# Kernel optimization log

Hardware: AMD Instinct MI355X
Metric: run time of the kernel (lower is better)

The kernel has to match this reference:

```python
import jax, jax.numpy as jnp
import numpy as np

# B=batch, S=seq_len, E=events per example, H=hidden, V=vocab
B, S, E, H, V = 16, 512, 32, 768, 50265


def setup_inputs() -> dict:
    key = jax.random.key(0)
    ks = jax.random.split(key, 12)
    batch_arg = jax.random.randint(ks[0], (B, S), 0, V)
    # distinct event positions per row (the torch loop visits each event once)
    event_pos = jax.vmap(lambda k: jax.random.permutation(k, S)[:E])(
        jax.random.split(ks[1], B))
    mask_indices = event_pos[:, 0]  # ensure the extracted token saw the fusion
    sent_emb = jax.random.normal(ks[2], (B, E, H), dtype=jnp.float32)
    type_emb = jax.random.normal(ks[3], (B, S, H), dtype=jnp.float32)
    emb_table = jax.random.normal(ks[4], (V, H), dtype=jnp.float32) * 0.02
    W1_1 = jax.random.normal(ks[5], (H, H), dtype=jnp.float32) * 0.02
    W1_2 = jax.random.normal(ks[6], (H, H), dtype=jnp.float32) * 0.02
    W2_1 = jax.random.normal(ks[7], (H, H), dtype=jnp.float32) * 0.02
    W2_2 = jax.random.normal(ks[8], (H, H), dtype=jnp.float32) * 0.02
    lm_W = jax.random.normal(ks[9], (H, V), dtype=jnp.float32) * 0.02
    lm_b = jnp.zeros((V,), dtype=jnp.float32)
    return dict(batch_arg=batch_arg, event_pos=event_pos,
                mask_indices=mask_indices, sent_emb=sent_emb,
                type_emb=type_emb, emb_table=emb_table,
                W1_1=W1_1, W1_2=W1_2, W2_1=W2_1, W2_2=W2_2,
                lm_W=lm_W, lm_b=lm_b)


def reference(batch_arg, event_pos, mask_indices, sent_emb, type_emb,
              emb_table, W1_1, W1_2, W2_1, W2_2, lm_W, lm_b):
    # word embedding lookup: [B,S,H]
    word_emb = emb_table[batch_arg]
    bidx = jnp.arange(B)[:, None]
    # gather per-event instance / type embeddings: [B,E,H]
    inst = word_emb[bidx, event_pos]
    typ = type_emb[bidx, event_pos]
    # gate 1: fuse instance with sentence embedding
    g1 = jax.nn.sigmoid(inst @ W1_1 + sent_emb @ W1_2)
    o1 = g1 * inst + (1.0 - g1) * sent_emb
    # gate 2: fuse with type embedding
    g2 = jax.nn.sigmoid(o1 @ W2_1 + typ @ W2_2)
    o2 = g2 * o1 + (1.0 - g2) * typ
    # scatter fused embeddings back into word_emb (positions are distinct)
    word_emb = word_emb.at[bidx, event_pos].set(o2)
    # extract mask-token embedding per example, project to vocab (lm_head)
    mask_emb = word_emb[jnp.arange(B), mask_indices]  # [B,H]
    prediction = mask_emb @ lm_W + lm_b  # [B,V]
    return prediction
```

## Files before the change

### kernel.cpp

```cpp
#include <hip/hip_runtime.h>

#define Hn 768
#define Bn 16
#define Sn 512
#define En 32
#define Vn 50265

#define WPB 8
#define KPW (Hn / WPB)
#define VPB 128
#define CH  4

__global__ __launch_bounds__(256) void gate_layer1(
    const int* __restrict__ batch_arg, const int* __restrict__ event_pos,
    const int* __restrict__ mask_indices, const float* __restrict__ sent_emb,
    const float* __restrict__ emb_table, const float* __restrict__ W1_1,
    const float* __restrict__ W1_2, float* __restrict__ o1_out)
{
    const int b  = blockIdx.x;
    const int j0 = threadIdx.x & 63;
    const int ks = threadIdx.x >> 6;
    const int j  = blockIdx.y * 64 + j0;

    const int mask = mask_indices[b];
    int estar = -1;
    #pragma unroll
    for (int e = 0; e < En; ++e)
        if (event_pos[b * En + e] == mask && estar < 0) estar = e;
    const int tok = batch_arg[b * Sn + mask];

    __shared__ __align__(16) float s_inst[Hn];
    __shared__ __align__(16) float s_sent[Hn];
    for (int t = threadIdx.x; t < Hn; t += 256) {
        s_inst[t] = emb_table[(size_t)tok * Hn + t];
        s_sent[t] = (estar >= 0) ? sent_emb[((size_t)b * En + estar) * Hn + t] : 0.f;
    }
    __syncthreads();

    float a0 = 0.f, a1 = 0.f, c0 = 0.f, c1 = 0.f;
    const float* __restrict__ w1 = W1_1 + (size_t)ks * 192 * Hn + j;
    const float* __restrict__ w2 = W1_2 + (size_t)ks * 192 * Hn + j;
    const float4* __restrict__ si = (const float4*)(s_inst + ks * 192);
    const float4* __restrict__ ss = (const float4*)(s_sent + ks * 192);
    #pragma unroll 4
    for (int k4 = 0; k4 < 48; ++k4) {
        const float4 iv = si[k4];
        const float4 sv = ss[k4];
        const float* __restrict__ wa = w1 + (size_t)k4 * 4 * Hn;
        const float* __restrict__ wb = w2 + (size_t)k4 * 4 * Hn;
        a0 = fmaf(iv.x, wa[0],      a0);
        a1 = fmaf(iv.y, wa[Hn],     a1);
        a0 = fmaf(iv.z, wa[2 * Hn], a0);
        a1 = fmaf(iv.w, wa[3 * Hn], a1);
        c0 = fmaf(sv.x, wb[0],      c0);
        c1 = fmaf(sv.y, wb[Hn],     c1);
        c0 = fmaf(sv.z, wb[2 * Hn], c0);
        c1 = fmaf(sv.w, wb[3 * Hn], c1);
    }

    __shared__ float r_a[4][64];
    __shared__ float r_c[4][64];
    r_a[ks][j0] = a0 + a1; r_c[ks][j0] = c0 + c1;
    __syncthreads();
    if (ks == 0) {
        const float A = r_a[0][j0] + r_a[1][j0] + r_a[2][j0] + r_a[3][j0];
        const float C = r_c[0][j0] + r_c[1][j0] + r_c[2][j0] + r_c[3][j0];
        const float g = 1.f / (1.f + expf(-(A + C)));
        o1_out[b * Hn + j] = g * s_inst[j] + (1.f - g) * s_sent[j];
    }
}

__global__ __launch_bounds__(256) void gate_layer2(
    const int* __restrict__ batch_arg, const int* __restrict__ event_pos,
    const int* __restrict__ mask_indices, const float* __restrict__ type_emb,
    const float* __restrict__ emb_table, const float* __restrict__ W2_1,
    const float* __restrict__ W2_2, const float* __restrict__ o1_in,
    float* __restrict__ me_t)
{
    const int b  = blockIdx.x;
    const int j0 = threadIdx.x & 63;
    const int ks = threadIdx.x >> 6;
    const int j  = blockIdx.y * 64 + j0;

    const int mask = mask_indices[b];
    int estar = -1;
    #pragma unroll
    for (int e = 0; e < En; ++e)
        if (event_pos[b * En + e] == mask && estar < 0) estar = e;
    const int tok = batch_arg[b * Sn + mask];

    __shared__ __align__(16) float s_o1[Hn];
    __shared__ __align__(16) float s_typ[Hn];
    for (int t = threadIdx.x; t < Hn; t += 256) {
        s_o1[t]  = o1_in[b * Hn + t];
        s_typ[t] = type_emb[((size_t)b * Sn + mask) * Hn + t];
    }
    __syncthreads();

    float a0 = 0.f, a1 = 0.f, c0 = 0.f, c1 = 0.f;
    const float* __restrict__ w1 = W2_1 + (size_t)ks * 192 * Hn + j;
    const float* __restrict__ w2 = W2_2 + (size_t)ks * 192 * Hn + j;
    const float4* __restrict__ so = (const float4*)(s_o1  + ks * 192);
    const float4* __restrict__ st = (const float4*)(s_typ + ks * 192);
    #pragma unroll 4
    for (int k4 = 0; k4 < 48; ++k4) {
        const float4 ov = so[k4];
        const float4 tv = st[k4];
        const float* __restrict__ wa = w1 + (size_t)k4 * 4 * Hn;
        const float* __restrict__ wb = w2 + (size_t)k4 * 4 * Hn;
        a0 = fmaf(ov.x, wa[0],      a0);
        a1 = fmaf(ov.y, wa[Hn],     a1);
        a0 = fmaf(ov.z, wa[2 * Hn], a0);
        a1 = fmaf(ov.w, wa[3 * Hn], a1);
        c0 = fmaf(tv.x, wb[0],      c0);
        c1 = fmaf(tv.y, wb[Hn],     c1);
        c0 = fmaf(tv.z, wb[2 * Hn], c0);
        c1 = fmaf(tv.w, wb[3 * Hn], c1);
    }

    __shared__ float r_a[4][64];
    __shared__ float r_c[4][64];
    r_a[ks][j0] = a0 + a1; r_c[ks][j0] = c0 + c1;
    __syncthreads();
    if (ks == 0) {
        const float A = r_a[0][j0] + r_a[1][j0] + r_a[2][j0] + r_a[3][j0];
        const float C = r_c[0][j0] + r_c[1][j0] + r_c[2][j0] + r_c[3][j0];
        const float g = 1.f / (1.f + expf(-(A + C)));
        float o2 = g * s_o1[j] + (1.f - g) * s_typ[j];
        if (estar < 0) o2 = emb_table[(size_t)tok * Hn + j];
        me_t[j * Bn + b] = o2;
    }
}

__global__ __launch_bounds__(512, 2) void lm_head(
    const float* __restrict__ me_t, const float* __restrict__ lm_W,
    const float* __restrict__ lm_b, float* __restrict__ out)
{
    __shared__ __align__(16) float smem[WPB * Bn * VPB];

    const int tid  = threadIdx.x;
    const int lane = tid & 63;
    const int w    = tid >> 6;
    const int bh   = lane & 1;
    const int vq   = lane >> 1;
    const int v0   = blockIdx.x * VPB + vq * 4;

    {
        const float4* __restrict__ src = (const float4*)me_t;
        float4* __restrict__ dst = (float4*)smem;
        #pragma unroll
        for (int i = 0; i < 6; ++i)
            dst[i * 512 + tid] = src[i * 512 + tid];
    }
    __syncthreads();

    const int kb = w * KPW;
    float4 acc[8];
    #pragma unroll
    for (int i = 0; i < 8; ++i) acc[i] = make_float4(0.f, 0.f, 0.f, 0.f);

    const float* __restrict__ mb = smem + kb * Bn + bh * 8;

#define FMA32(wv, m0, m1)                                                     \
    acc[0].x = fmaf(m0.x, wv.x, acc[0].x); acc[0].y = fmaf(m0.x, wv.y, acc[0].y); \
    acc[0].z = fmaf(m0.x, wv.z, acc[0].z); acc[0].w = fmaf(m0.x, wv.w, acc[0].w); \
    acc[1].x = fmaf(m0.y, wv.x, acc[1].x); acc[1].y = fmaf(m0.y, wv.y, acc[1].y); \
    acc[1].z = fmaf(m0.y, wv.z, acc[1].z); acc[1].w = fmaf(m0.y, wv.w, acc[1].w); \
    acc[2].x = fmaf(m0.z, wv.x, acc[2].x); acc[2].y = fmaf(m0.z, wv.y, acc[2].y); \
    acc[2].z = fmaf(m0.z, wv.z, acc[2].z); acc[2].w = fmaf(m0.z, wv.w, acc[2].w); \
    acc[3].x = fmaf(m0.w, wv.x, acc[3].x); acc[3].y = fmaf(m0.w, wv.y, acc[3].y); \
    acc[3].z = fmaf(m0.w, wv.z, acc[3].z); acc[3].w = fmaf(m0.w, wv.w, acc[3].w); \
    acc[4].x = fmaf(m1.x, wv.x, acc[4].x); acc[4].y = fmaf(m1.x, wv.y, acc[4].y); \
    acc[4].z = fmaf(m1.x, wv.z, acc[4].z); acc[4].w = fmaf(m1.x, wv.w, acc[4].w); \
    acc[5].x = fmaf(m1.y, wv.x, acc[5].x); acc[5].y = fmaf(m1.y, wv.y, acc[5].y); \
    acc[5].z = fmaf(m1.y, wv.z, acc[5].z); acc[5].w = fmaf(m1.y, wv.w, acc[5].w); \
    acc[6].x = fmaf(m1.z, wv.x, acc[6].x); acc[6].y = fmaf(m1.z, wv.y, acc[6].y); \
    acc[6].z = fmaf(m1.z, wv.z, acc[6].z); acc[6].w = fmaf(m1.z, wv.w, acc[6].w); \
    acc[7].x = fmaf(m1.w, wv.x, acc[7].x); acc[7].y = fmaf(m1.w, wv.y, acc[7].y); \
    acc[7].z = fmaf(m1.w, wv.z, acc[7].z); acc[7].w = fmaf(m1.w, wv.w, acc[7].w);

    if (__all(v0 + 3 < Vn)) {
        const float* __restrict__ wp = lm_W + (size_t)kb * Vn + v0;
        float4 cur[CH], nxt[CH];
        #pragma unroll
        for (int u = 0; u < CH; ++u)
            cur[u] = *(const float4*)(wp + (size_t)u * Vn);

        for (int k0 = 0; k0 < KPW; k0 += CH) {
            if (k0 + CH < KPW) {
                #pragma unroll
                for (int u = 0; u < CH; ++u)
                    nxt[u] = *(const float4*)(wp + (size_t)(k0 + CH + u) * Vn);
            }
            #pragma unroll
            for (int u = 0; u < CH; ++u) {
                const float4 wv = cur[u];
                const float4 m0 = *(const float4*)(mb + (k0 + u) * Bn);
                const float4 m1 = *(const float4*)(mb + (k0 + u) * Bn + 4);
                FMA32(wv, m0, m1)
            }
            #pragma unroll
            for (int u = 0; u < CH; ++u) cur[u] = nxt[u];
        }
    } else {
        const float* __restrict__ wq = lm_W + (size_t)kb * Vn;
        const int vx0 = (v0     < Vn) ? v0     : (Vn - 1);
        const int vx1 = (v0 + 1 < Vn) ? v0 + 1 : (Vn - 1);
        const int vx2 = (v0 + 2 < Vn) ? v0 + 2 : (Vn - 1);
        const int vx3 = (v0 + 3 < Vn) ? v0 + 3 : (Vn - 1);
        for (int k = 0; k < KPW; ++k) {
            float4 wv;
            wv.x = wq[(size_t)k * Vn + vx0];
            wv.y = wq[(size_t)k * Vn + vx1];
            wv.z = wq[(size_t)k * Vn + vx2];
            wv.w = wq[(size_t)k * Vn + vx3];
            const float4 m0 = *(const float4*)(mb + k * Bn);
            const float4 m1 = *(const float4*)(mb + k * Bn + 4);
            FMA32(wv, m0, m1)
        }
    }
#undef FMA32

    __syncthreads();
    #pragma unroll
    for (int i = 0; i < 8; ++i)
        *(float4*)&smem[((w * Bn) + bh * 8 + i) * VPB + vq * 4] = acc[i];
    __syncthreads();

    #pragma unroll
    for (int p0 = 0; p0 < 4; ++p0) {
        const int p  = p0 * 512 + tid;
        const int b  = p >> 7;
        const int l  = p & 127;
        const int vv = blockIdx.x * VPB + l;
        if (vv < Vn) {
            float s = 0.f;
            #pragma unroll
            for (int ww = 0; ww < WPB; ++ww) s += smem[(ww * Bn + b) * VPB + l];
            out[(size_t)b * Vn + vv] = s + lm_b[vv];
        }
    }
}

extern "C" void kernel_launch(void* const* d_in, const int* in_sizes, int n_in,
                              void* d_out, int out_size, void* d_ws, size_t ws_size,
                              hipStream_t stream) {
    const int*   batch_arg    = (const int*)  d_in[0];
    const int*   event_pos    = (const int*)  d_in[1];
    const int*   mask_indices = (const int*)  d_in[2];
    const float* sent_emb     = (const float*)d_in[3];
    const float* type_emb     = (const float*)d_in[4];
    const float* emb_table    = (const float*)d_in[5];
    const float* W1_1         = (const float*)d_in[6];
    const float* W1_2         = (const float*)d_in[7];
    const float* W2_1         = (const float*)d_in[8];
    const float* W2_2         = (const float*)d_in[9];
    const float* lm_W         = (const float*)d_in[10];
    const float* lm_b         = (const float*)d_in[11];
    float* out = (float*)d_out;

    float* o1_ws = (float*)d_ws;
    float* me_t  = o1_ws + (size_t)Bn * Hn;

    dim3 g12(Bn, Hn / 64);
    gate_layer1<<<g12, 256, 0, stream>>>(batch_arg, event_pos, mask_indices,
                                         sent_emb, emb_table, W1_1, W1_2, o1_ws);
    gate_layer2<<<g12, 256, 0, stream>>>(batch_arg, event_pos, mask_indices,
                                         type_emb, emb_table, W2_1, W2_2, o1_ws, me_t);

    lm_head<<<(Vn + VPB - 1) / VPB, 512, 0, stream>>>(me_t, lm_W, lm_b, out);
}
```

Measured before the change: 65.97 us.

## Split lm_head across K chunks with atomic accumulation and bias-init kernel

```diff
diff --git a/kernel.cpp b/kernel.cpp
--- a/kernel.cpp
+++ b/kernel.cpp
@@ -6,10 +6,17 @@
 #define En 32
 #define Vn 50265
 
-#define WPB 8
-#define KPW (Hn / WPB)
-#define VPB 128
-#define CH  4
+#define KC   4
+#define KPC  (Hn / KC)
+#define KPW  (KPC / 4)
+#define VPB  128
+
+__global__ __launch_bounds__(256) void out_init(
+    const float* __restrict__ lm_b, float* __restrict__ out)
+{
+    const int v = blockIdx.x * 256 + threadIdx.x;
+    if (v < Vn) out[(size_t)blockIdx.y * Vn + v] = lm_b[v];
+}
 
 __global__ __launch_bounds__(256) void gate_layer1(
     const int* __restrict__ batch_arg, const int* __restrict__ event_pos,
@@ -132,34 +139,36 @@
     }
 }
 
-__global__ __launch_bounds__(512, 2) void lm_head(
+__global__ __launch_bounds__(256) void lm_head_splitk(
     const float* __restrict__ me_t, const float* __restrict__ lm_W,
-    const float* __restrict__ lm_b, float* __restrict__ out)
-{
-    __shared__ __align__(16) float smem[WPB * Bn * VPB];
+    float* __restrict__ out)
+{
+    __shared__ __align__(16) float s_me[KPC * Bn];
+    __shared__ __align__(16) float red[4][8][VPB];
 
     const int tid  = threadIdx.x;
     const int lane = tid & 63;
     const int w    = tid >> 6;
     const int bh   = lane & 1;
     const int vq   = lane >> 1;
+    const int kc   = blockIdx.y;
     const int v0   = blockIdx.x * VPB + vq * 4;
 
     {
-        const float4* __restrict__ src = (const float4*)me_t;
-        float4* __restrict__ dst = (float4*)smem;
+        const float4* __restrict__ src = (const float4*)(me_t + kc * KPC * Bn);
+        float4* __restrict__ dst = (float4*)s_me;
         #pragma unroll
-        for (int i = 0; i < 6; ++i)
-            dst[i * 512 + tid] = src[i * 512 + tid];
-    }
-    __syncthreads();
-
-    const int kb = w * KPW;
+        for (int i = 0; i < 3; ++i)
+            dst[i * 256 + tid] = src[i * 256 + tid];
+    }
+    __syncthreads();
+
+    const int kb = kc * KPC + w * KPW;
     float4 acc[8];
     #pragma unroll
     for (int i = 0; i < 8; ++i) acc[i] = make_float4(0.f, 0.f, 0.f, 0.f);
 
-    const float* __restrict__ mb = smem + kb * Bn + bh * 8;
+    const float* __restrict__ mb = s_me + (w * KPW) * Bn + bh * 8;
 
 #define FMA32(wv, m0, m1)                                                     \
     acc[0].x = fmaf(m0.x, wv.x, acc[0].x); acc[0].y = fmaf(m0.x, wv.y, acc[0].y); \
@@ -181,26 +190,12 @@
 
     if (__all(v0 + 3 < Vn)) {
         const float* __restrict__ wp = lm_W + (size_t)kb * Vn + v0;
-        float4 cur[CH], nxt[CH];
-        #pragma unroll
-        for (int u = 0; u < CH; ++u)
-            cur[u] = *(const float4*)(wp + (size_t)u * Vn);
-
-        for (int k0 = 0; k0 < KPW; k0 += CH) {
-            if (k0 + CH < KPW) {
-                #pragma unroll
-                for (int u = 0; u < CH; ++u)
-                    nxt[u] = *(const float4*)(wp + (size_t)(k0 + CH + u) * Vn);
-            }
-            #pragma unroll
-            for (int u = 0; u < CH; ++u) {
-                const float4 wv = cur[u];
-                const float4 m0 = *(const float4*)(mb + (k0 + u) * Bn);
-                const float4 m1 = *(const float4*)(mb + (k0 + u) * Bn + 4);
-                FMA32(wv, m0, m1)
-            }
-            #pragma unroll
-            for (int u = 0; u < CH; ++u) cur[u] = nxt[u];
+        #pragma unroll 4
+        for (int k = 0; k < KPW; ++k) {
+            const float4 wv = *(const float4*)(wp + (size_t)k * Vn);
+            const float4 m0 = *(const float4*)(mb + k * Bn);
+            const float4 m1 = *(const float4*)(mb + k * Bn + 4);
+            FMA32(wv, m0, m1)
         }
     } else {
         const float* __restrict__ wq = lm_W + (size_t)kb * Vn;
@@ -221,23 +216,26 @@
     }
 #undef FMA32
 
-    __syncthreads();
-    #pragma unroll
-    for (int i = 0; i < 8; ++i)
-        *(float4*)&smem[((w * Bn) + bh * 8 + i) * VPB + vq * 4] = acc[i];
-    __syncthreads();
-
-    #pragma unroll
-    for (int p0 = 0; p0 < 4; ++p0) {
-        const int p  = p0 * 512 + tid;
-        const int b  = p >> 7;
-        const int l  = p & 127;
-        const int vv = blockIdx.x * VPB + l;
-        if (vv < Vn) {
-            float s = 0.f;
+    #pragma unroll
+    for (int half = 0; half < 2; ++half) {
+        __syncthreads();
+        if (bh == half) {
             #pragma unroll
-            for (int ww = 0; ww < WPB; ++ww) s += smem[(ww * Bn + b) * VPB + l];
-            out[(size_t)b * Vn + vv] = s + lm_b[vv];
+            for (int i = 0; i < 8; ++i)
+                *(float4*)&red[w][i][vq * 4] = acc[i];
+        }
+        __syncthreads();
+        #pragma unroll
+        for (int e = 0; e < 4; ++e) {
+            const int j  = tid * 4 + e;
+            const int bb = (j >> 7) + half * 8;
+            const int l  = j & 127;
+            const int vv = blockIdx.x * VPB + l;
+            if (vv < Vn) {
+                const float s = red[0][j >> 7][l] + red[1][j >> 7][l]
+                              + red[2][j >> 7][l] + red[3][j >> 7][l];
+                atomicAdd(&out[(size_t)bb * Vn + vv], s);
+            }
         }
     }
 }
@@ -262,11 +260,15 @@
     float* o1_ws = (float*)d_ws;
     float* me_t  = o1_ws + (size_t)Bn * Hn;
 
+    dim3 gv((Vn + 255) / 256, Bn);
+    out_init<<<gv, 256, 0, stream>>>(lm_b, out);
+
     dim3 g12(Bn, Hn / 64);
     gate_layer1<<<g12, 256, 0, stream>>>(batch_arg, event_pos, mask_indices,
                                          sent_emb, emb_table, W1_1, W1_2, o1_ws);
     gate_layer2<<<g12, 256, 0, stream>>>(batch_arg, event_pos, mask_indices,
                                          type_emb, emb_table, W2_1, W2_2, o1_ws, me_t);
 
-    lm_head<<<(Vn + VPB - 1) / VPB, 512, 0, stream>>>(me_t, lm_W, lm_b, out);
-}
+    dim3 gh((Vn + VPB - 1) / VPB, KC);
+    lm_head_splitk<<<gh, 256, 0, stream>>>(me_t, lm_W, out);
+}
```

After: 96.59 us. 1.46x slower.
